# Kernel tuning notes

Hardware: AMD Instinct MI355X
Metric: run time of the kernel (lower is better)

## Reference

```python
import jax, jax.numpy as jnp
import numpy as np

H = 8  # GRU hidden size (Dimension)


def _gru_last_hidden(x, Wih, Whh, bih, bhh):
    """Torch-style GRU (batch_first), returns final hidden state [B, H].
    x: [B, T, In]; Wih: [3H, In]; Whh: [3H, H]; bih, bhh: [3H].
    Gate order (torch): r, z, n.
    """
    B = x.shape[0]
    # precompute input projections for all timesteps: [B, T, 3H]
    xg = jnp.einsum('bti,gi->btg', x, Wih) + bih

    def step(h, xt):  # h: [B,H], xt: [B,3H]
        gh = h @ Whh.T + bhh  # [B, 3H]
        xr, xz, xn = jnp.split(xt, 3, axis=-1)
        hr, hz, hn = jnp.split(gh, 3, axis=-1)
        r = jax.nn.sigmoid(xr + hr)
        z = jax.nn.sigmoid(xz + hz)
        n = jnp.tanh(xn + r * hn)
        h_new = (1.0 - z) * n + z * h
        return h_new, None

    h0 = jnp.zeros((B, H), dtype=x.dtype)
    hT, _ = jax.lax.scan(step, h0, jnp.swapaxes(xg, 0, 1))  # scan over T
    return hT


def setup_inputs() -> dict:
    key = jax.random.key(0)
    ks = jax.random.split(key, 10)
    B, T = 1024, 512
    s = 0.2  # param init scale ~ 1/sqrt(H)*... small
    return {
        'bbox': jax.random.normal(ks[0], (B, T, 4), dtype=jnp.float32),
        'flow': jax.random.normal(ks[1], (B, T, 5, 5, 2), dtype=jnp.float32),
        'Wih_b': jax.random.normal(ks[2], (3 * H, 4), dtype=jnp.float32) * s,
        'Whh_b': jax.random.normal(ks[3], (3 * H, H), dtype=jnp.float32) * s,
        'bih_b': jax.random.normal(ks[4], (3 * H,), dtype=jnp.float32) * s,
        'bhh_b': jax.random.normal(ks[5], (3 * H,), dtype=jnp.float32) * s,
        'Wih_f': jax.random.normal(ks[6], (3 * H, 2), dtype=jnp.float32) * s,
        'Whh_f': jax.random.normal(ks[7], (3 * H, H), dtype=jnp.float32) * s,
        'bih_f': jax.random.normal(ks[8], (3 * H,), dtype=jnp.float32) * s,
        'bhh_f': jax.random.normal(ks[9], (3 * H,), dtype=jnp.float32) * s,
    }


def reference(bbox, flow, Wih_b, Whh_b, bih_b, bhh_b, Wih_f, Whh_f, bih_f, bhh_f):
    # vectorized equivalent of the triple Python loop: take center pixel
    storage = flow[:, :, 2, 2, :]  # [B, T, 2]
    h_bbox = _gru_last_hidden(bbox, Wih_b, Whh_b, bih_b, bhh_b)      # [B, H]
    h_flow = _gru_last_hidden(storage, Wih_f, Whh_f, bih_f, bhh_f)   # [B, H]
    feature = (h_bbox + h_flow) * 0.5
    return feature
```

## Files before the change

### kernel.cpp

```cpp
#include <hip/hip_runtime.h>

#define HDIM 8
#define CHUNK 16

__device__ __forceinline__ float ex2(float x) {
#if __has_builtin(__builtin_amdgcn_exp2f)
    return __builtin_amdgcn_exp2f(x);
#else
    return exp2f(x);
#endif
}
__device__ __forceinline__ float rcp(float x) {
#if __has_builtin(__builtin_amdgcn_rcpf)
    return __builtin_amdgcn_rcpf(x);
#else
    return 1.0f / x;
#endif
}

#define DPP_ROR(v, N)                                                        \
    __int_as_float(__builtin_amdgcn_update_dpp(                              \
        0, __float_as_int(v), 0x120 + (N), 0xF, 0xF, true))


template <int IN, int STRIDE>
__device__ __forceinline__ void produce_chunk(
    const float* __restrict__ xb, int t0,
    const float (&ur)[4], const float (&uz)[4], const float (&un)[4],
    float cr, float cz, float cn,
    float4* __restrict__ dst, int lane)
{
#pragma unroll
    for (int h = 0; h < 2; ++h) {
        float xs[8][IN];
#pragma unroll
        for (int s = 0; s < 8; ++s) {
            const float* p = xb + (size_t)(t0 + h * 8 + s) * STRIDE;
            if constexpr (IN == 4) {
                float4 v = *reinterpret_cast<const float4*>(p);
                xs[s][0] = v.x; xs[s][1] = v.y; xs[s][2] = v.z; xs[s][3] = v.w;
            } else {
                float2 v = *reinterpret_cast<const float2*>(p);
                xs[s][0] = v.x; xs[s][1] = v.y;
            }
        }
#pragma unroll
        for (int s = 0; s < 8; ++s) {
            float a = cr, b = cz, c = cn;
#pragma unroll
            for (int i = 0; i < IN; ++i) {
                a = fmaf(ur[i], xs[s][i], a);
                b = fmaf(uz[i], xs[s][i], b);
                c = fmaf(un[i], xs[s][i], c);
            }
            dst[(h * 8 + s) * 64 + lane] = make_float4(a, b, c, 0.0f);
        }
    }
}

__device__ __forceinline__ float consume_chunk(
    float hj, const float4* __restrict__ src, int lane,
    const float (&wr)[8], const float (&wz)[8], const float (&wn)[8], float bhn)
{
    float4 pf[4];
    pf[0] = src[0 * 64 + lane];
    pf[1] = src[1 * 64 + lane];
    pf[2] = src[2 * 64 + lane];
#pragma unroll
    for (int s = 0; s < CHUNK; ++s) {
        if (s + 3 < CHUNK) pf[(s + 3) & 3] = src[(s + 3) * 64 + lane];
        const float4 P = pf[s & 3];

        const float hx0 = hj;
        const float hx1 = DPP_ROR(hj,  2);
        const float hx2 = DPP_ROR(hj,  4);
        const float hx3 = DPP_ROR(hj,  6);
        const float hx4 = DPP_ROR(hj,  8);
        const float hx5 = DPP_ROR(hj, 10);
        const float hx6 = DPP_ROR(hj, 12);
        const float hx7 = DPP_ROR(hj, 14);

        float r01 = fmaf(wr[1], hx1, fmaf(wr[0], hx0, P.x));
        float r23 = fmaf(wr[3], hx3, wr[2] * hx2);
        float r45 = fmaf(wr[5], hx5, wr[4] * hx4);
        float r67 = fmaf(wr[7], hx7, wr[6] * hx6);
        float z01 = fmaf(wz[1], hx1, fmaf(wz[0], hx0, P.y));
        float z23 = fmaf(wz[3], hx3, wz[2] * hx2);
        float z45 = fmaf(wz[5], hx5, wz[4] * hx4);
        float z67 = fmaf(wz[7], hx7, wz[6] * hx6);
        float n01 = fmaf(wn[1], hx1, fmaf(wn[0], hx0, bhn));
        float n23 = fmaf(wn[3], hx3, wn[2] * hx2);
        float n45 = fmaf(wn[5], hx5, wn[4] * hx4);
        float n67 = fmaf(wn[7], hx7, wn[6] * hx6);
        float sr = (r01 + r23) + (r45 + r67);
        float sz = (z01 + z23) + (z45 + z67);
        float sn = (n01 + n23) + (n45 + n67);

        float r = rcp(1.0f + ex2(sr));
        float z = rcp(1.0f + ex2(sz));
        float u = fmaf(r, sn, P.z);
        float n = fmaf(-2.0f, rcp(1.0f + ex2(u)), 1.0f);
        hj = fmaf(z, hj - n, n);
    }
    return hj;
}

__global__ __launch_bounds__(256, 1)
void gru_fused_kernel(const float* __restrict__ bbox, const float* __restrict__ flow,
                      const float* __restrict__ Wih_b, const float* __restrict__ Whh_b,
                      const float* __restrict__ bih_b, const float* __restrict__ bhh_b,
                      const float* __restrict__ Wih_f, const float* __restrict__ Whh_f,
                      const float* __restrict__ bih_f, const float* __restrict__ bhh_f,
                      float* __restrict__ out, int T)
{
    const float NL2E = -1.4426950408889634f;
    const float L2E2 =  2.8853900817779268f;

    __shared__ float4 projLDS[2][2][CHUNK * 64];
    __shared__ float sh[2][8][HDIM];

    const int tid  = threadIdx.x;
    const int wave = tid >> 6;
    const int lane = tid & 63;
    const int gru  = wave & 1;
    const bool is_cons = (wave < 2);
    const int NC = T / CHUNK;

    const int eloc = ((lane >> 4) << 1) | (lane & 1);
    const int j    = (lane & 15) >> 1;

    float wr[8], wz[8], wn[8];
    float bhn = 0.0f;
    float ur[4] = {0, 0, 0, 0}, uz[4] = {0, 0, 0, 0}, un[4] = {0, 0, 0, 0};
    float cr = 0.0f, cz = 0.0f, cn = 0.0f;
    const float* pxb = nullptr;

    if (is_cons) {
        const float* Whh = gru ? Whh_f : Whh_b;
        const float* bhh = gru ? bhh_f : bhh_b;
        float nbp = DPP_ROR((float)j, 2);
        const int dstep = (nbp == (float)((j + 1) & 7)) ? 1 : 7;
#pragma unroll
        for (int m = 0; m < 8; ++m) {
            const int k = (j + dstep * m) & 7;
            wr[m] = NL2E * Whh[(j     ) * HDIM + k];
            wz[m] = NL2E * Whh[(j +  8) * HDIM + k];
            wn[m] = L2E2 * Whh[(j + 16) * HDIM + k];
        }
        bhn = L2E2 * bhh[j + 16];
    } else {
        const float* Wih = gru ? Wih_f : Wih_b;
        const float* bih = gru ? bih_f : bih_b;
        const float* bhh = gru ? bhh_f : bhh_b;
        const int IN = gru ? 2 : 4;
        const int pe = blockIdx.x * 8 + eloc;
        pxb = gru ? (flow + (size_t)pe * T * 50 + 24)
                  : (bbox + (size_t)pe * T * 4);
        for (int i = 0; i < IN; ++i) {
            ur[i] = NL2E * Wih[(j     ) * IN + i];
            uz[i] = NL2E * Wih[(j +  8) * IN + i];
            un[i] = L2E2 * Wih[(j + 16) * IN + i];
        }
        cr = NL2E * (bih[j]     + bhh[j]);
        cz = NL2E * (bih[j + 8] + bhh[j + 8]);
        cn = L2E2 * bih[j + 16];
    }

    float hj = 0.0f;

    if (!is_cons) {
        float4* dst = projLDS[0][gru];
        if (gru == 0) produce_chunk<4, 4 >(pxb, 0, ur, uz, un, cr, cz, cn, dst, lane);
        else          produce_chunk<2, 50>(pxb, 0, ur, uz, un, cr, cz, cn, dst, lane);
    }
    __syncthreads();

    for (int c = 0; c < NC; ++c) {
        if (is_cons) {
            hj = consume_chunk(hj, projLDS[c & 1][gru], lane, wr, wz, wn, bhn);
        } else if (c + 1 < NC) {
            float4* dst = projLDS[(c + 1) & 1][gru];
            if (gru == 0) produce_chunk<4, 4 >(pxb, (c + 1) * CHUNK, ur, uz, un, cr, cz, cn, dst, lane);
            else          produce_chunk<2, 50>(pxb, (c + 1) * CHUNK, ur, uz, un, cr, cz, cn, dst, lane);
        }
        __syncthreads();
    }

    if (is_cons) sh[gru][eloc][j] = hj;
    __syncthreads();
    if (wave == 0) {
        const int e = blockIdx.x * 8 + eloc;
        out[(size_t)e * HDIM + j] = 0.5f * (sh[0][eloc][j] + sh[1][eloc][j]);
    }
}

extern "C" void kernel_launch(void* const* d_in, const int* in_sizes, int n_in,
                              void* d_out, int out_size, void* d_ws, size_t ws_size,
                              hipStream_t stream) {
    const float* bbox  = (const float*)d_in[0];
    const float* flow  = (const float*)d_in[1];
    const float* Wih_b = (const float*)d_in[2];
    const float* Whh_b = (const float*)d_in[3];
    const float* bih_b = (const float*)d_in[4];
    const float* bhh_b = (const float*)d_in[5];
    const float* Wih_f = (const float*)d_in[6];
    const float* Whh_f = (const float*)d_in[7];
    const float* bih_f = (const float*)d_in[8];
    const float* bhh_f = (const float*)d_in[9];
    float* out = (float*)d_out;

    const int B = out_size / HDIM;
    const int T = in_sizes[0] / (4 * B);

    dim3 grid(B / 8), block(256);
    gru_fused_kernel<<<grid, block, 0, stream>>>(
        bbox, flow, Wih_b, Whh_b, bih_b, bhh_b,
        Wih_f, Whh_f, bih_f, bhh_f, out, T);
}
```

Before: 62.46 us.

## Pack r/z gate matvec into packed FMA and preload whole chunk from LDS

The r and z gate dot products against the hidden state are computed with two-wide vector FMAs, so the compiler can emit packed fp32 FMA instructions that handle both gates at once. This cuts the per-step instruction count on the serial recurrence. Separately, all sixteen per-step projections of a chunk are loaded from LDS up front rather than through a rolling three-deep prefetch. The trade-off is higher register pressure and a changed summation order for the r/z accumulators.

```diff
diff --git a/kernel.cpp b/kernel.cpp
--- a/kernel.cpp
+++ b/kernel.cpp
@@ -2,6 +2,8 @@
 
 #define HDIM 8
 #define CHUNK 16
+
+typedef float v2f __attribute__((ext_vector_type(2)));
 
 __device__ __forceinline__ float ex2(float x) {
 #if __has_builtin(__builtin_amdgcn_exp2f)
@@ -60,16 +62,15 @@
 
 __device__ __forceinline__ float consume_chunk(
     float hj, const float4* __restrict__ src, int lane,
-    const float (&wr)[8], const float (&wz)[8], const float (&wn)[8], float bhn)
+    const v2f (&wrz)[8], const float (&wn)[8], float bhn)
 {
-    float4 pf[4];
-    pf[0] = src[0 * 64 + lane];
-    pf[1] = src[1 * 64 + lane];
-    pf[2] = src[2 * 64 + lane];
+    float4 Pb[CHUNK];
+#pragma unroll
+    for (int s = 0; s < CHUNK; ++s) Pb[s] = src[s * 64 + lane];
+
 #pragma unroll
     for (int s = 0; s < CHUNK; ++s) {
-        if (s + 3 < CHUNK) pf[(s + 3) & 3] = src[(s + 3) * 64 + lane];
-        const float4 P = pf[s & 3];
+        const float4 P = Pb[s];
 
         const float hx0 = hj;
         const float hx1 = DPP_ROR(hj,  2);
@@ -80,24 +81,25 @@
         const float hx6 = DPP_ROR(hj, 12);
         const float hx7 = DPP_ROR(hj, 14);
 
-        float r01 = fmaf(wr[1], hx1, fmaf(wr[0], hx0, P.x));
-        float r23 = fmaf(wr[3], hx3, wr[2] * hx2);
-        float r45 = fmaf(wr[5], hx5, wr[4] * hx4);
-        float r67 = fmaf(wr[7], hx7, wr[6] * hx6);
-        float z01 = fmaf(wz[1], hx1, fmaf(wz[0], hx0, P.y));
-        float z23 = fmaf(wz[3], hx3, wz[2] * hx2);
-        float z45 = fmaf(wz[5], hx5, wz[4] * hx4);
-        float z67 = fmaf(wz[7], hx7, wz[6] * hx6);
+        v2f accA = { P.x, P.y };
+        accA = __builtin_elementwise_fma((v2f){hx0, hx0}, wrz[0], accA);
+        accA = __builtin_elementwise_fma((v2f){hx1, hx1}, wrz[1], accA);
+        accA = __builtin_elementwise_fma((v2f){hx2, hx2}, wrz[2], accA);
+        accA = __builtin_elementwise_fma((v2f){hx3, hx3}, wrz[3], accA);
+        v2f accB = (v2f){hx4, hx4} * wrz[4];
+        accB = __builtin_elementwise_fma((v2f){hx5, hx5}, wrz[5], accB);
+        accB = __builtin_elementwise_fma((v2f){hx6, hx6}, wrz[6], accB);
+        accB = __builtin_elementwise_fma((v2f){hx7, hx7}, wrz[7], accB);
+        v2f srz = accA + accB;
+
         float n01 = fmaf(wn[1], hx1, fmaf(wn[0], hx0, bhn));
         float n23 = fmaf(wn[3], hx3, wn[2] * hx2);
         float n45 = fmaf(wn[5], hx5, wn[4] * hx4);
         float n67 = fmaf(wn[7], hx7, wn[6] * hx6);
-        float sr = (r01 + r23) + (r45 + r67);
-        float sz = (z01 + z23) + (z45 + z67);
         float sn = (n01 + n23) + (n45 + n67);
 
-        float r = rcp(1.0f + ex2(sr));
-        float z = rcp(1.0f + ex2(sz));
+        float r = rcp(1.0f + ex2(srz.x));
+        float z = rcp(1.0f + ex2(srz.y));
         float u = fmaf(r, sn, P.z);
         float n = fmaf(-2.0f, rcp(1.0f + ex2(u)), 1.0f);
         hj = fmaf(z, hj - n, n);
@@ -129,7 +131,8 @@
     const int eloc = ((lane >> 4) << 1) | (lane & 1);
     const int j    = (lane & 15) >> 1;
 
-    float wr[8], wz[8], wn[8];
+    v2f wrz[8];
+    float wn[8];
     float bhn = 0.0f;
     float ur[4] = {0, 0, 0, 0}, uz[4] = {0, 0, 0, 0}, un[4] = {0, 0, 0, 0};
     float cr = 0.0f, cz = 0.0f, cn = 0.0f;
@@ -143,9 +146,9 @@
 #pragma unroll
         for (int m = 0; m < 8; ++m) {
             const int k = (j + dstep * m) & 7;
-            wr[m] = NL2E * Whh[(j     ) * HDIM + k];
-            wz[m] = NL2E * Whh[(j +  8) * HDIM + k];
-            wn[m] = L2E2 * Whh[(j + 16) * HDIM + k];
+            wrz[m] = (v2f){ NL2E * Whh[(j    ) * HDIM + k],
+                            NL2E * Whh[(j + 8) * HDIM + k] };
+            wn[m]  = L2E2 * Whh[(j + 16) * HDIM + k];
         }
         bhn = L2E2 * bhh[j + 16];
     } else {
@@ -177,7 +180,7 @@
 
     for (int c = 0; c < NC; ++c) {
         if (is_cons) {
-            hj = consume_chunk(hj, projLDS[c & 1][gru], lane, wr, wz, wn, bhn);
+            hj = consume_chunk(hj, projLDS[c & 1][gru], lane, wrz, wn, bhn);
         } else if (c + 1 < NC) {
             float4* dst = projLDS[(c + 1) & 1][gru];
             if (gru == 0) produce_chunk<4, 4 >(pxb, (c + 1) * CHUNK, ur, uz, un, cr, cz, cn, dst, lane);
```

Measured after the change: 61.02 us. 2.3% less time.
